# Kernel tuning notes

Measured on AMD Instinct MI355X. Metric: run time of the kernel, lower is better.

The kernel has to match this reference:

```python
import jax, jax.numpy as jnp
import numpy as np

PN = 1  # replication pad width for num_connected=9
OFFSETS = [(-1, -1), (-1, 0), (-1, 1), (0, -1), (0, 0), (0, 1), (1, -1), (1, 0), (1, 1)]
K = len(OFFSETS)


def setup_inputs() -> dict:
    key = jax.random.key(0)
    k1, k2, k3, k4 = jax.random.split(key, 4)
    B, Cin, Cv = 8, 128, 128
    H, W, I = 64, 64, 2
    guide = jax.random.normal(k1, (B, Cin, H * I, W * I), dtype=jnp.float32)
    value = jax.random.normal(k2, (B, Cv, H, W), dtype=jnp.float32)
    w_conv = jax.random.normal(k3, (K, Cin), dtype=jnp.float32) * 0.05  # 1x1 conv weight
    b_conv = jax.random.normal(k4, (K,), dtype=jnp.float32) * 0.05
    return {"guide": guide, "value": value, "w_conv": w_conv, "b_conv": b_conv}


def _make_offsets(x):
    # x: [B, C, H, W] -> [B, C, K, H, W] of replication-padded shifted neighbors
    B, C, H, W = x.shape
    xp = jnp.pad(x, ((0, 0), (0, 0), (PN, PN), (PN, PN)), mode="edge")
    slices = [xp[:, :, PN + o0:PN + o0 + H, PN + o1:PN + o1 + W] for (o0, o1) in OFFSETS]
    return jnp.stack(slices, axis=2)


def reference(guide, value, w_conv, b_conv):
    B, C, H, W = value.shape
    H_out, W_out = guide.shape[2], guide.shape[3]
    I = H_out // H
    # 1x1 conv: [B,Cin,Ho,Wo] x [K,Cin] -> [B,K,Ho,Wo]
    att = jnp.einsum("bchw,kc->bkhw", guide, w_conv) + b_conv[None, :, None, None]
    # conv_res=True, guide channels (Cin) > K: residual_auto adds guide[:, :K]
    att = guide[:, :K] + att
    att = jax.nn.softmax(att, axis=1)
    att = att.reshape(B, K, H, I, W, I)
    xk = _make_offsets(value)  # [B, C, K, H, W]
    # fused gather-multiply-reduce over the connection dim K
    res = jnp.einsum("bckhw,bkhiwj->bchiwj", xk, att)
    return res.reshape(B, C, H_out, W_out)
```

## Files before the change

### kernel.cpp

```cpp
#include <hip/hip_runtime.h>

#define NB 8
#define CH 128
#define HV 64
#define WV 64
#define HO 128
#define WO 128
#define KK 9

__global__ __launch_bounds__(256)
void la_att(const float* __restrict__ guide,
            const float* __restrict__ wconv,
            const float* __restrict__ bconv,
            float* __restrict__ att)
{
    const int tid = threadIdx.x;
    const int p  = blockIdx.x * 256 + tid;
    const int wo = p & 127;
    const int ho = (p >> 7) & 127;
    const int b  = p >> 14;

    const float* gpix = guide + ((size_t)b * CH) * (HO * WO) + ho * WO + wo;

    float a[KK];
    #pragma unroll
    for (int k = 0; k < KK; ++k)
        a[k] = bconv[k];

    #pragma unroll
    for (int c = 0; c < KK; ++c) {
        float g = gpix[(size_t)c * (HO * WO)];
        #pragma unroll
        for (int k = 0; k < KK; ++k)
            a[k] += g * wconv[k * CH + c];
        a[c] += g;
    }

    #pragma unroll 8
    for (int c = KK; c < CH; ++c) {
        float g = gpix[(size_t)c * (HO * WO)];
        #pragma unroll
        for (int k = 0; k < KK; ++k)
            a[k] += g * wconv[k * CH + c];
    }

    float m = a[0];
    #pragma unroll
    for (int k = 1; k < KK; ++k) m = fmaxf(m, a[k]);
    float s = 0.f;
    #pragma unroll
    for (int k = 0; k < KK; ++k) { a[k] = __expf(a[k] - m); s += a[k]; }
    float r = 1.0f / s;

    float* apix = att + ((size_t)b * KK) * (HO * WO) + ho * WO + wo;
    #pragma unroll
    for (int k = 0; k < KK; ++k)
        apix[(size_t)k * (HO * WO)] = a[k] * r;
}

#define CHUNK 8
__global__ __launch_bounds__(256)
void la_gather(const float* __restrict__ value,
               const float* __restrict__ att,
               float* __restrict__ out)
{
    const int tid   = threadIdx.x;
    const int lane  = tid & 63;
    const int wseq  = blockIdx.x * 4 + (tid >> 6);
    const int chunk = wseq & 15;
    const int h     = (wseq >> 4) & 63;
    const int b     = wseq >> 10;

    const int hm = (h > 0) ? h - 1 : 0;
    const int hp = (h < HV - 1) ? h + 1 : HV - 1;
    const float* vc  = value + ((size_t)b * CH + chunk * CHUNK) * (HV * WV) + lane;
    const float* prm = vc + hm * WV;
    const float* pr0 = vc + h  * WV;
    const float* prp = vc + hp * WV;

    float vm[CHUNK], v0[CHUNK], vp[CHUNK];
    #pragma unroll
    for (int cc = 0; cc < CHUNK; ++cc) {
        vm[cc] = prm[(size_t)cc * (HV * WV)];
        v0[cc] = pr0[(size_t)cc * (HV * WV)];
        vp[cc] = prp[(size_t)cc * (HV * WV)];
    }

    float a00[KK], a01[KK], a10[KK], a11[KK];
    {
        const float* ap = att + ((size_t)b * KK * HO + 2 * h) * WO + 2 * lane;
        #pragma unroll
        for (int k = 0; k < KK; ++k) {
            float2 r0 = *(const float2*)(ap + (size_t)k * (HO * WO));
            float2 r1 = *(const float2*)(ap + (size_t)k * (HO * WO) + WO);
            a00[k] = r0.x; a01[k] = r0.y;
            a10[k] = r1.x; a11[k] = r1.y;
        }
    }

    float* ob = out + (((size_t)b * CH + chunk * CHUNK) * HO + 2 * h) * WO + 2 * lane;

    #pragma unroll
    for (int cc = 0; cc < CHUNK; ++cc) {
        float tm = vm[cc], t0 = v0[cc], tp = vp[cc];
        float tmL = __shfl_up(tm, 1), tmR = __shfl_down(tm, 1);
        float t0L = __shfl_up(t0, 1), t0R = __shfl_down(t0, 1);
        float tpL = __shfl_up(tp, 1), tpR = __shfl_down(tp, 1);

        float s00 = tmL*a00[0] + tm*a00[1] + tmR*a00[2]
                  + t0L*a00[3] + t0*a00[4] + t0R*a00[5]
                  + tpL*a00[6] + tp*a00[7] + tpR*a00[8];
        float s01 = tmL*a01[0] + tm*a01[1] + tmR*a01[2]
                  + t0L*a01[3] + t0*a01[4] + t0R*a01[5]
                  + tpL*a01[6] + tp*a01[7] + tpR*a01[8];
        float s10 = tmL*a10[0] + tm*a10[1] + tmR*a10[2]
                  + t0L*a10[3] + t0*a10[4] + t0R*a10[5]
                  + tpL*a10[6] + tp*a10[7] + tpR*a10[8];
        float s11 = tmL*a11[0] + tm*a11[1] + tmR*a11[2]
                  + t0L*a11[3] + t0*a11[4] + t0R*a11[5]
                  + tpL*a11[6] + tp*a11[7] + tpR*a11[8];

        float* oc = ob + (size_t)cc * (HO * WO);
        float2 r0; r0.x = s00; r0.y = s01;
        float2 r1; r1.x = s10; r1.y = s11;
        *(float2*)oc        = r0;
        *(float2*)(oc + WO) = r1;
    }
}

#define CCH 8
__global__ __launch_bounds__(128)
void la_fused(const float* __restrict__ guide,
              const float* __restrict__ value,
              const float* __restrict__ wconv,
              const float* __restrict__ bconv,
              float* __restrict__ out)
{
    __shared__ float s_wT[CH * 12];
    __shared__ float s_haloF[CCH * 110];

    const int tid = threadIdx.x;
    const int blk = blockIdx.x;
    const int wt = blk & 7;
    const int ht = (blk >> 3) & 7;
    const int b  = blk >> 6;

    for (int i = tid; i < KK * CH; i += 128) {
        int k = i >> 7;
        int c = i & 127;
        s_wT[c * 12 + k] = wconv[i];
    }

    const int tlwp = tid & 7;
    const int tho  = tid >> 3;
    const int ho = ht * 16 + tho;
    const int wo = wt * 16 + tlwp * 2;

    const float* gpix = guide + (((size_t)b * CH) * HO + ho) * WO + wo;

    float att0[KK], att1[KK];
    #pragma unroll
    for (int k = 0; k < KK; ++k) {
        float2 g = *(const float2*)(gpix + (size_t)k * (HO * WO));
        float bc = bconv[k];
        att0[k] = bc + g.x;
        att1[k] = bc + g.y;
    }
    __syncthreads();

    #pragma unroll 4
    for (int c = 0; c < CH; ++c) {
        float2 g = *(const float2*)(gpix + (size_t)c * (HO * WO));
        const float4* wt4 = (const float4*)&s_wT[c * 12];
        float4 wa = wt4[0];
        float4 wb = wt4[1];
        float w8 = s_wT[c * 12 + 8];
        att0[0] += g.x * wa.x;  att1[0] += g.y * wa.x;
        att0[1] += g.x * wa.y;  att1[1] += g.y * wa.y;
        att0[2] += g.x * wa.z;  att1[2] += g.y * wa.z;
        att0[3] += g.x * wa.w;  att1[3] += g.y * wa.w;
        att0[4] += g.x * wb.x;  att1[4] += g.y * wb.x;
        att0[5] += g.x * wb.y;  att1[5] += g.y * wb.y;
        att0[6] += g.x * wb.z;  att1[6] += g.y * wb.z;
        att0[7] += g.x * wb.w;  att1[7] += g.y * wb.w;
        att0[8] += g.x * w8;    att1[8] += g.y * w8;
    }

    float m0 = att0[0], m1 = att1[0];
    #pragma unroll
    for (int k = 1; k < KK; ++k) { m0 = fmaxf(m0, att0[k]); m1 = fmaxf(m1, att1[k]); }
    float s0 = 0.f, s1 = 0.f;
    #pragma unroll
    for (int k = 0; k < KK; ++k) {
        att0[k] = __expf(att0[k] - m0); s0 += att0[k];
        att1[k] = __expf(att1[k] - m1); s1 += att1[k];
    }
    float r0 = 1.0f / s0, r1 = 1.0f / s1;
    #pragma unroll
    for (int k = 0; k < KK; ++k) { att0[k] *= r0; att1[k] *= r1; }

    const int h0 = ht * 8 - 1;
    const int w0 = wt * 8 - 1;
    const int lh = tho >> 1;
    const float* vb = value + (size_t)b * CH * (HV * WV);
    float* ob = out + (((size_t)b * CH) * HO + ho) * WO + wo;

    for (int c0 = 0; c0 < CH; c0 += CCH) {
        __syncthreads();
        for (int i = tid; i < CCH * 100; i += 128) {
            int cc = i / 100;
            int r  = i - cc * 100;
            int hr = r / 10;
            int wr = r - hr * 10;
            int hh = min(max(h0 + hr, 0), HV - 1);
            int ww = min(max(w0 + wr, 0), WV - 1);
            s_haloF[cc * 110 + hr * 11 + wr] =
                vb[(size_t)(c0 + cc) * (HV * WV) + hh * WV + ww];
        }
        __syncthreads();
        #pragma unroll
        for (int cc = 0; cc < CCH; ++cc) {
            const float* hp = &s_haloF[cc * 110 + lh * 11 + tlwp];
            float v, q0, q1;
            v = hp[0];  q0  = v * att0[0]; q1  = v * att1[0];
            v = hp[1];  q0 += v * att0[1]; q1 += v * att1[1];
            v = hp[2];  q0 += v * att0[2]; q1 += v * att1[2];
            v = hp[11]; q0 += v * att0[3]; q1 += v * att1[3];
            v = hp[12]; q0 += v * att0[4]; q1 += v * att1[4];
            v = hp[13]; q0 += v * att0[5]; q1 += v * att1[5];
            v = hp[22]; q0 += v * att0[6]; q1 += v * att1[6];
            v = hp[23]; q0 += v * att0[7]; q1 += v * att1[7];
            v = hp[24]; q0 += v * att0[8]; q1 += v * att1[8];
            float2 rr; rr.x = q0; rr.y = q1;
            *(float2*)(ob + (size_t)(c0 + cc) * (HO * WO)) = rr;
        }
    }
}

extern "C" void kernel_launch(void* const* d_in, const int* in_sizes, int n_in,
                              void* d_out, int out_size, void* d_ws, size_t ws_size,
                              hipStream_t stream) {
    const float* guide = (const float*)d_in[0];
    const float* value = (const float*)d_in[1];
    const float* wconv = (const float*)d_in[2];
    const float* bconv = (const float*)d_in[3];
    float* outp = (float*)d_out;
    (void)in_sizes; (void)n_in; (void)out_size;

    const size_t att_bytes = (size_t)NB * KK * HO * WO * sizeof(float);
    if (ws_size >= att_bytes) {
        float* attp = (float*)d_ws;
        la_att<<<dim3(512), dim3(256), 0, stream>>>(guide, wconv, bconv, attp);
        la_gather<<<dim3(2048), dim3(256), 0, stream>>>(value, attp, outp);
    } else {
        la_fused<<<dim3(NB * 8 * 8), dim3(128), 0, stream>>>(guide, value, wconv, bconv, outp);
    }
}
```

Baseline: 156.2 us.

## Fuse attention softmax and gather into one kernel using shared-memory attention

Replaces the two-kernel path (attention written to a workspace, then a gather kernel) with one kernel per (batch, value row). Each block computes softmax attention for two output rows into shared memory, then four wavefronts each handle 32 channels of the neighbour gather. This removes the round trip of the attention tensor through global memory and one launch. In exchange the grid drops to 512 blocks, each doing more serial channel work, so parallelism is lower.

```diff
diff --git a/kernel.cpp b/kernel.cpp
--- a/kernel.cpp
+++ b/kernel.cpp
@@ -8,231 +8,122 @@
 #define WO 128
 #define KK 9
 
+#define SATT 10
 __global__ __launch_bounds__(256)
-void la_att(const float* __restrict__ guide,
-            const float* __restrict__ wconv,
-            const float* __restrict__ bconv,
-            float* __restrict__ att)
+void la_fused2(const float* __restrict__ guide,
+               const float* __restrict__ value,
+               const float* __restrict__ wconv,
+               const float* __restrict__ bconv,
+               float* __restrict__ out)
 {
+    __shared__ float s_att[256 * SATT];
+
     const int tid = threadIdx.x;
-    const int p  = blockIdx.x * 256 + tid;
-    const int wo = p & 127;
-    const int ho = (p >> 7) & 127;
-    const int b  = p >> 14;
+    const int blk = blockIdx.x;
+    const int h   = blk & 63;
+    const int b   = blk >> 6;
 
-    const float* gpix = guide + ((size_t)b * CH) * (HO * WO) + ho * WO + wo;
+    {
+        const int col = tid & 127;
+        const int row = 2 * h + (tid >> 7);
+        const float* gpix = guide + ((size_t)b * CH) * (HO * WO) + row * WO + col;
 
-    float a[KK];
-    #pragma unroll
-    for (int k = 0; k < KK; ++k)
-        a[k] = bconv[k];
-
-    #pragma unroll
-    for (int c = 0; c < KK; ++c) {
-        float g = gpix[(size_t)c * (HO * WO)];
+        float a[KK];
         #pragma unroll
         for (int k = 0; k < KK; ++k)
-            a[k] += g * wconv[k * CH + c];
-        a[c] += g;
+            a[k] = bconv[k];
+
+        #pragma unroll
+        for (int c = 0; c < KK; ++c) {
+            float g = gpix[(size_t)c * (HO * WO)];
+            #pragma unroll
+            for (int k = 0; k < KK; ++k)
+                a[k] += g * wconv[k * CH + c];
+            a[c] += g;
+        }
+        #pragma unroll 8
+        for (int c = KK; c < CH; ++c) {
+            float g = gpix[(size_t)c * (HO * WO)];
+            #pragma unroll
+            for (int k = 0; k < KK; ++k)
+                a[k] += g * wconv[k * CH + c];
+        }
+
+        float m = a[0];
+        #pragma unroll
+        for (int k = 1; k < KK; ++k) m = fmaxf(m, a[k]);
+        float s = 0.f;
+        #pragma unroll
+        for (int k = 0; k < KK; ++k) { a[k] = __expf(a[k] - m); s += a[k]; }
+        float r = 1.0f / s;
+
+        float* ap = &s_att[tid * SATT];
+        #pragma unroll
+        for (int k = 0; k < KK; ++k)
+            ap[k] = a[k] * r;
     }
 
-    #pragma unroll 8
-    for (int c = KK; c < CH; ++c) {
-        float g = gpix[(size_t)c * (HO * WO)];
+    __syncthreads();
+
+    const int lane = tid & 63;
+    const int wv   = tid >> 6;
+
+    float a00[KK], a01[KK], a10[KK], a11[KK];
+    {
+        const float* p00 = &s_att[(2 * lane) * SATT];
+        const float* p01 = &s_att[(2 * lane + 1) * SATT];
+        const float* p10 = &s_att[(128 + 2 * lane) * SATT];
+        const float* p11 = &s_att[(128 + 2 * lane + 1) * SATT];
         #pragma unroll
-        for (int k = 0; k < KK; ++k)
-            a[k] += g * wconv[k * CH + c];
+        for (int k = 0; k < KK; ++k) {
+            a00[k] = p00[k]; a01[k] = p01[k];
+            a10[k] = p10[k]; a11[k] = p11[k];
+        }
     }
-
-    float m = a[0];
-    #pragma unroll
-    for (int k = 1; k < KK; ++k) m = fmaxf(m, a[k]);
-    float s = 0.f;
-    #pragma unroll
-    for (int k = 0; k < KK; ++k) { a[k] = __expf(a[k] - m); s += a[k]; }
-    float r = 1.0f / s;
-
-    float* apix = att + ((size_t)b * KK) * (HO * WO) + ho * WO + wo;
-    #pragma unroll
-    for (int k = 0; k < KK; ++k)
-        apix[(size_t)k * (HO * WO)] = a[k] * r;
-}
-
-#define CHUNK 8
-__global__ __launch_bounds__(256)
-void la_gather(const float* __restrict__ value,
-               const float* __restrict__ att,
-               float* __restrict__ out)
-{
-    const int tid   = threadIdx.x;
-    const int lane  = tid & 63;
-    const int wseq  = blockIdx.x * 4 + (tid >> 6);
-    const int chunk = wseq & 15;
-    const int h     = (wseq >> 4) & 63;
-    const int b     = wseq >> 10;
 
     const int hm = (h > 0) ? h - 1 : 0;
     const int hp = (h < HV - 1) ? h + 1 : HV - 1;
-    const float* vc  = value + ((size_t)b * CH + chunk * CHUNK) * (HV * WV) + lane;
+    const int cbase = wv * 32;
+    const float* vc  = value + ((size_t)b * CH + cbase) * (HV * WV) + lane;
     const float* prm = vc + hm * WV;
     const float* pr0 = vc + h  * WV;
     const float* prp = vc + hp * WV;
+    float* ob = out + (((size_t)b * CH + cbase) * HO + 2 * h) * WO + 2 * lane;
 
-    float vm[CHUNK], v0[CHUNK], vp[CHUNK];
-    #pragma unroll
-    for (int cc = 0; cc < CHUNK; ++cc) {
-        vm[cc] = prm[(size_t)cc * (HV * WV)];
-        v0[cc] = pr0[(size_t)cc * (HV * WV)];
-        vp[cc] = prp[(size_t)cc * (HV * WV)];
-    }
+    for (int c4 = 0; c4 < 32; c4 += 4) {
+        float vm[4], v0[4], vp[4];
+        #pragma unroll
+        for (int j = 0; j < 4; ++j) {
+            size_t off = (size_t)(c4 + j) * (HV * WV);
+            vm[j] = prm[off];
+            v0[j] = pr0[off];
+            vp[j] = prp[off];
+        }
+        #pragma unroll
+        for (int j = 0; j < 4; ++j) {
+            float tm = vm[j], t0 = v0[j], tp = vp[j];
+            float tmL = __shfl_up(tm, 1), tmR = __shfl_down(tm, 1);
+            float t0L = __shfl_up(t0, 1), t0R = __shfl_down(t0, 1);
+            float tpL = __shfl_up(tp, 1), tpR = __shfl_down(tp, 1);
 
-    float a00[KK], a01[KK], a10[KK], a11[KK];
-    {
-        const float* ap = att + ((size_t)b * KK * HO + 2 * h) * WO + 2 * lane;
-        #pragma unroll
-        for (int k = 0; k < KK; ++k) {
-            float2 r0 = *(const float2*)(ap + (size_t)k * (HO * WO));
-            float2 r1 = *(const float2*)(ap + (size_t)k * (HO * WO) + WO);
-            a00[k] = r0.x; a01[k] = r0.y;
-            a10[k] = r1.x; a11[k] = r1.y;
-        }
-    }
+            float s00 = tmL*a00[0] + tm*a00[1] + tmR*a00[2]
+                      + t0L*a00[3] + t0*a00[4] + t0R*a00[5]
+                      + tpL*a00[6] + tp*a00[7] + tpR*a00[8];
+            float s01 = tmL*a01[0] + tm*a01[1] + tmR*a01[2]
+                      + t0L*a01[3] + t0*a01[4] + t0R*a01[5]
+                      + tpL*a01[6] + tp*a01[7] + tpR*a01[8];
+            float s10 = tmL*a10[0] + tm*a10[1] + tmR*a10[2]
+                      + t0L*a10[3] + t0*a10[4] + t0R*a10[5]
+                      + tpL*a10[6] + tp*a10[7] + tpR*a10[8];
+            float s11 = tmL*a11[0] + tm*a11[1] + tmR*a11[2]
+                      + t0L*a11[3] + t0*a11[4] + t0R*a11[5]
+                      + tpL*a11[6] + tp*a11[7] + tpR*a11[8];
 
-    float* ob = out + (((size_t)b * CH + chunk * CHUNK) * HO + 2 * h) * WO + 2 * lane;
-
-    #pragma unroll
-    for (int cc = 0; cc < CHUNK; ++cc) {
-        float tm = vm[cc], t0 = v0[cc], tp = vp[cc];
-        float tmL = __shfl_up(tm, 1), tmR = __shfl_down(tm, 1);
-        float t0L = __shfl_up(t0, 1), t0R = __shfl_down(t0, 1);
-        float tpL = __shfl_up(tp, 1), tpR = __shfl_down(tp, 1);
-
-        float s00 = tmL*a00[0] + tm*a00[1] + tmR*a00[2]
-                  + t0L*a00[3] + t0*a00[4] + t0R*a00[5]
-                  + tpL*a00[6] + tp*a00[7] + tpR*a00[8];
-        float s01 = tmL*a01[0] + tm*a01[1] + tmR*a01[2]
-                  + t0L*a01[3] + t0*a01[4] + t0R*a01[5]
-                  + tpL*a01[6] + tp*a01[7] + tpR*a01[8];
-        float s10 = tmL*a10[0] + tm*a10[1] + tmR*a10[2]
-                  + t0L*a10[3] + t0*a10[4] + t0R*a10[5]
-                  + tpL*a10[6] + tp*a10[7] + tpR*a10[8];
-        float s11 = tmL*a11[0] + tm*a11[1] + tmR*a11[2]
-                  + t0L*a11[3] + t0*a11[4] + t0R*a11[5]
-                  + tpL*a11[6] + tp*a11[7] + tpR*a11[8];
-
-        float* oc = ob + (size_t)cc * (HO * WO);
-        float2 r0; r0.x = s00; r0.y = s01;
-        float2 r1; r1.x = s10; r1.y = s11;
-        *(float2*)oc        = r0;
-        *(float2*)(oc + WO) = r1;
-    }
-}
-
-#define CCH 8
-__global__ __launch_bounds__(128)
-void la_fused(const float* __restrict__ guide,
-              const float* __restrict__ value,
-              const float* __restrict__ wconv,
-              const float* __restrict__ bconv,
-              float* __restrict__ out)
-{
-    __shared__ float s_wT[CH * 12];
-    __shared__ float s_haloF[CCH * 110];
-
-    const int tid = threadIdx.x;
-    const int blk = blockIdx.x;
-    const int wt = blk & 7;
-    const int ht = (blk >> 3) & 7;
-    const int b  = blk >> 6;
-
-    for (int i = tid; i < KK * CH; i += 128) {
-        int k = i >> 7;
-        int c = i & 127;
-        s_wT[c * 12 + k] = wconv[i];
-    }
-
-    const int tlwp = tid & 7;
-    const int tho  = tid >> 3;
-    const int ho = ht * 16 + tho;
-    const int wo = wt * 16 + tlwp * 2;
-
-    const float* gpix = guide + (((size_t)b * CH) * HO + ho) * WO + wo;
-
-    float att0[KK], att1[KK];
-    #pragma unroll
-    for (int k = 0; k < KK; ++k) {
-        float2 g = *(const float2*)(gpix + (size_t)k * (HO * WO));
-        float bc = bconv[k];
-        att0[k] = bc + g.x;
-        att1[k] = bc + g.y;
-    }
-    __syncthreads();
-
-    #pragma unroll 4
-    for (int c = 0; c < CH; ++c) {
-        float2 g = *(const float2*)(gpix + (size_t)c * (HO * WO));
-        const float4* wt4 = (const float4*)&s_wT[c * 12];
-        float4 wa = wt4[0];
-        float4 wb = wt4[1];
-        float w8 = s_wT[c * 12 + 8];
-        att0[0] += g.x * wa.x;  att1[0] += g.y * wa.x;
-        att0[1] += g.x * wa.y;  att1[1] += g.y * wa.y;
-        att0[2] += g.x * wa.z;  att1[2] += g.y * wa.z;
-        att0[3] += g.x * wa.w;  att1[3] += g.y * wa.w;
-        att0[4] += g.x * wb.x;  att1[4] += g.y * wb.x;
-        att0[5] += g.x * wb.y;  att1[5] += g.y * wb.y;
-        att0[6] += g.x * wb.z;  att1[6] += g.y * wb.z;
-        att0[7] += g.x * wb.w;  att1[7] += g.y * wb.w;
-        att0[8] += g.x * w8;    att1[8] += g.y * w8;
-    }
-
-    float m0 = att0[0], m1 = att1[0];
-    #pragma unroll
-    for (int k = 1; k < KK; ++k) { m0 = fmaxf(m0, att0[k]); m1 = fmaxf(m1, att1[k]); }
-    float s0 = 0.f, s1 = 0.f;
-    #pragma unroll
-    for (int k = 0; k < KK; ++k) {
-        att0[k] = __expf(att0[k] - m0); s0 += att0[k];
-        att1[k] = __expf(att1[k] - m1); s1 += att1[k];
-    }
-    float r0 = 1.0f / s0, r1 = 1.0f / s1;
-    #pragma unroll
-    for (int k = 0; k < KK; ++k) { att0[k] *= r0; att1[k] *= r1; }
-
-    const int h0 = ht * 8 - 1;
-    const int w0 = wt * 8 - 1;
-    const int lh = tho >> 1;
-    const float* vb = value + (size_t)b * CH * (HV * WV);
-    float* ob = out + (((size_t)b * CH) * HO + ho) * WO + wo;
-
-    for (int c0 = 0; c0 < CH; c0 += CCH) {
-        __syncthreads();
-        for (int i = tid; i < CCH * 100; i += 128) {
-            int cc = i / 100;
-            int r  = i - cc * 100;
-            int hr = r / 10;
-            int wr = r - hr * 10;
-            int hh = min(max(h0 + hr, 0), HV - 1);
-            int ww = min(max(w0 + wr, 0), WV - 1);
-            s_haloF[cc * 110 + hr * 11 + wr] =
-                vb[(size_t)(c0 + cc) * (HV * WV) + hh * WV + ww];
-        }
-        __syncthreads();
-        #pragma unroll
-        for (int cc = 0; cc < CCH; ++cc) {
-            const float* hp = &s_haloF[cc * 110 + lh * 11 + tlwp];
-            float v, q0, q1;
-            v = hp[0];  q0  = v * att0[0]; q1  = v * att1[0];
-            v = hp[1];  q0 += v * att0[1]; q1 += v * att1[1];
-            v = hp[2];  q0 += v * att0[2]; q1 += v * att1[2];
-            v = hp[11]; q0 += v * att0[3]; q1 += v * att1[3];
-            v = hp[12]; q0 += v * att0[4]; q1 += v * att1[4];
-            v = hp[13]; q0 += v * att0[5]; q1 += v * att1[5];
-            v = hp[22]; q0 += v * att0[6]; q1 += v * att1[6];
-            v = hp[23]; q0 += v * att0[7]; q1 += v * att1[7];
-            v = hp[24]; q0 += v * att0[8]; q1 += v * att1[8];
-            float2 rr; rr.x = q0; rr.y = q1;
-            *(float2*)(ob + (size_t)(c0 + cc) * (HO * WO)) = rr;
+            float* oc = ob + (size_t)(c4 + j) * (HO * WO);
+            float2 r0; r0.x = s00; r0.y = s01;
+            float2 r1; r1.x = s10; r1.y = s11;
+            *(float2*)oc        = r0;
+            *(float2*)(oc + WO) = r1;
         }
     }
 }
@@ -245,14 +136,7 @@
     const float* wconv = (const float*)d_in[2];
     const float* bconv = (const float*)d_in[3];
     float* outp = (float*)d_out;
-    (void)in_sizes; (void)n_in; (void)out_size;
+    (void)in_sizes; (void)n_in; (void)out_size; (void)d_ws; (void)ws_size;
 
-    const size_t att_bytes = (size_t)NB * KK * HO * WO * sizeof(float);
-    if (ws_size >= att_bytes) {
-        float* attp = (float*)d_ws;
-        la_att<<<dim3(512), dim3(256), 0, stream>>>(guide, wconv, bconv, attp);
-        la_gather<<<dim3(2048), dim3(256), 0, stream>>>(value, attp, outp);
-    } else {
-        la_fused<<<dim3(NB * 8 * 8), dim3(128), 0, stream>>>(guide, value, wconv, bconv, outp);
-    }
+    la_fused2<<<dim3(NB * HV), dim3(256), 0, stream>>>(guide, value, wconv, bconv, outp);
 }
```

Result: slower. 175.2 us (+12.2%).

## Split attention conv channel reduction across four waves with shared-memory combine

Applied to the files above, without the earlier changes.

The attention kernel now gives each pixel to four waves, each summing a quarter of the 128 guide channels, instead of one thread looping over all channels. Partial sums are combined through shared memory, and the first wave then does the bias, softmax and store. The grid grows from 512 to 2048 blocks to expose more memory-level parallelism on the guide read, which dominates traffic. The cost is a block barrier, extra LDS traffic, and three of four waves idling during the softmax phase.

```diff
diff --git a/kernel.cpp b/kernel.cpp
--- a/kernel.cpp
+++ b/kernel.cpp
@@ -8,14 +8,19 @@
 #define WO 128
 #define KK 9
 
+#define ASTR 40
 __global__ __launch_bounds__(256)
 void la_att(const float* __restrict__ guide,
             const float* __restrict__ wconv,
             const float* __restrict__ bconv,
             float* __restrict__ att)
 {
+    __shared__ float s_part[64 * ASTR];
+
     const int tid = threadIdx.x;
-    const int p  = blockIdx.x * 256 + tid;
+    const int lpx = tid & 63;
+    const int q   = tid >> 6;
+    const int p   = blockIdx.x * 64 + lpx;
     const int wo = p & 127;
     const int ho = (p >> 7) & 127;
     const int b  = p >> 14;
@@ -24,38 +29,61 @@
 
     float a[KK];
     #pragma unroll
-    for (int k = 0; k < KK; ++k)
-        a[k] = bconv[k];
-
-    #pragma unroll
-    for (int c = 0; c < KK; ++c) {
-        float g = gpix[(size_t)c * (HO * WO)];
+    for (int k = 0; k < KK; ++k) a[k] = 0.f;
+
+    if (q == 0) {
+        #pragma unroll
+        for (int c = 0; c < KK; ++c) {
+            float g = gpix[(size_t)c * (HO * WO)];
+            #pragma unroll
+            for (int k = 0; k < KK; ++k)
+                a[k] += g * wconv[k * CH + c];
+            a[c] += g;
+        }
+        #pragma unroll 8
+        for (int c = KK; c < 32; ++c) {
+            float g = gpix[(size_t)c * (HO * WO)];
+            #pragma unroll
+            for (int k = 0; k < KK; ++k)
+                a[k] += g * wconv[k * CH + c];
+        }
+    } else {
+        const int cbeg = q * 32;
+        #pragma unroll 8
+        for (int c0 = 0; c0 < 32; ++c0) {
+            float g = gpix[(size_t)(cbeg + c0) * (HO * WO)];
+            #pragma unroll
+            for (int k = 0; k < KK; ++k)
+                a[k] += g * wconv[k * CH + cbeg + c0];
+        }
+    }
+
+    float* sp = &s_part[lpx * ASTR + q];
+    #pragma unroll
+    for (int k = 0; k < KK; ++k) sp[k * 4] = a[k];
+    __syncthreads();
+
+    if (tid < 64) {
+        const float* rp = &s_part[lpx * ASTR];
+        float v[KK];
+        #pragma unroll
+        for (int k = 0; k < KK; ++k) {
+            float4 t = *(const float4*)(rp + k * 4);
+            v[k] = bconv[k] + t.x + t.y + t.z + t.w;
+        }
+        float m = v[0];
+        #pragma unroll
+        for (int k = 1; k < KK; ++k) m = fmaxf(m, v[k]);
+        float s = 0.f;
+        #pragma unroll
+        for (int k = 0; k < KK; ++k) { v[k] = __expf(v[k] - m); s += v[k]; }
+        float r = 1.0f / s;
+
+        float* apix = att + ((size_t)b * KK) * (HO * WO) + ho * WO + wo;
         #pragma unroll
         for (int k = 0; k < KK; ++k)
-            a[k] += g * wconv[k * CH + c];
-        a[c] += g;
-    }
-
-    #pragma unroll 8
-    for (int c = KK; c < CH; ++c) {
-        float g = gpix[(size_t)c * (HO * WO)];
-        #pragma unroll
-        for (int k = 0; k < KK; ++k)
-            a[k] += g * wconv[k * CH + c];
-    }
-
-    float m = a[0];
-    #pragma unroll
-    for (int k = 1; k < KK; ++k) m = fmaxf(m, a[k]);
-    float s = 0.f;
-    #pragma unroll
-    for (int k = 0; k < KK; ++k) { a[k] = __expf(a[k] - m); s += a[k]; }
-    float r = 1.0f / s;
-
-    float* apix = att + ((size_t)b * KK) * (HO * WO) + ho * WO + wo;
-    #pragma unroll
-    for (int k = 0; k < KK; ++k)
-        apix[(size_t)k * (HO * WO)] = a[k] * r;
+            apix[(size_t)k * (HO * WO)] = v[k] * r;
+    }
 }
 
 #define CHUNK 8
@@ -250,7 +278,7 @@
     const size_t att_bytes = (size_t)NB * KK * HO * WO * sizeof(float);
     if (ws_size >= att_bytes) {
         float* attp = (float*)d_ws;
-        la_att<<<dim3(512), dim3(256), 0, stream>>>(guide, wconv, bconv, attp);
+        la_att<<<dim3(2048), dim3(256), 0, stream>>>(guide, wconv, bconv, attp);
         la_gather<<<dim3(2048), dim3(256), 0, stream>>>(value, attp, outp);
     } else {
         la_fused<<<dim3(NB * 8 * 8), dim3(128), 0, stream>>>(guide, value, wconv, bconv, outp);
```

Result: no change. 153.6 us (-1.7%).
